# Optimization experiments

Hardware: AMD Instinct MI355X
Metric: run time of the kernel (lower is better)

## Reference

```python
import jax, jax.numpy as jnp
import numpy as np


def binarize(x):
    # sign-binarization to {-1, +1}; zeros map to -1, matching torch.where(tensor > 0, 1, -1)
    return jnp.where(x > 0, jnp.float32(1.0), jnp.float32(-1.0))


def setup_inputs() -> dict:
    key = jax.random.key(0)
    k1, k2, k3 = jax.random.split(key, 3)
    N, IN, OUT = 8192, 4096, 4096
    input = jax.random.normal(k1, (N, IN), dtype=jnp.float32)
    weight = jax.random.normal(k2, (IN, OUT), dtype=jnp.float32)  # [in_features, out_features]
    bias = jax.random.normal(k3, (OUT,), dtype=jnp.float32)
    return {"input": input, "weight": weight, "bias": bias}


def reference(input, weight, bias):
    # Binarize activations; quantized_weight is the binarized weight.
    x_b = binarize(input)            # [N, in]
    w_b = binarize(weight)           # [in, out]
    # XNOR/popcount GEMM over +-1 operands == plain matmul of the sign matrices.
    out = jnp.matmul(x_b, w_b) + bias  # [N, out]
    return out
```

## Files before the change

### kernel.cpp

```cpp
#include <hip/hip_runtime.h>
#include <stdint.h>


#define N_ROWS 8192
#define K_DIM  4096
#define O_DIM  4096
#define KW     64

typedef int   int4v    __attribute__((ext_vector_type(4)));
typedef int   int8v    __attribute__((ext_vector_type(8)));
typedef float float16v __attribute__((ext_vector_type(16)));

__device__ __forceinline__ int8v mk8u(int4v x) {
    return __builtin_shufflevector(x, x, 0, 1, 2, 3, -1, -1, -1, -1);
}

__device__ __forceinline__ uint32_t nib4(float f) { return f > 0.0f ? 0x2u : 0xAu; }

__global__ __launch_bounds__(256) void convert_xw_fp4(
        const float* __restrict__ X, const float* __restrict__ W,
        uint8_t* __restrict__ XB, uint8_t* __restrict__ WB) {
    int u    = blockIdx.x * 4 + (threadIdx.x >> 6);
    int lane = threadIdx.x & 63;

    if (u < 16384) {
        int g = u & 7, kt = (u >> 3) & 63, G = u >> 9;
        int row = G * 256 + g * 32 + (lane & 31);
        int k0  = kt * 64 + (lane >> 5) * 32;
        const float4* src = (const float4*)(X + (size_t)row * K_DIM + k0);
        uint32_t ow[4];
        #pragma unroll
        for (int q = 0; q < 4; ++q) {
            float4 vA = src[2 * q];
            float4 vB = src[2 * q + 1];
            uint32_t b0 = nib4(vA.x) | (nib4(vA.y) << 4);
            uint32_t b1 = nib4(vA.z) | (nib4(vA.w) << 4);
            uint32_t b2 = nib4(vB.x) | (nib4(vB.y) << 4);
            uint32_t b3 = nib4(vB.z) | (nib4(vB.w) << 4);
            ow[q] = b0 | (b1 << 8) | (b2 << 16) | (b3 << 24);
        }
        int4v o; o.x = (int)ow[0]; o.y = (int)ow[1]; o.z = (int)ow[2]; o.w = (int)ow[3];
        *(int4v*)(XB + (size_t)u * 1024 + lane * 16) = o;
    } else {
        int v = u - 16384;
        int g = v & 7, kt = (v >> 3) & 63, G = v >> 9;
        int o     = G * 256 + g * 32 + (lane & 31);
        int kbase = kt * 64 + (lane >> 5) * 32;
        const float* src = W + (size_t)kbase * O_DIM + o;
        uint32_t ow[4];
        #pragma unroll
        for (int q = 0; q < 4; ++q) {
            uint32_t x = 0;
            #pragma unroll
            for (int j = 0; j < 8; ++j) {
                float f = src[(size_t)(q * 8 + j) * O_DIM];
                x |= nib4(f) << (4 * j);
            }
            ow[q] = x;
        }
        int4v ov; ov.x = (int)ow[0]; ov.y = (int)ow[1]; ov.z = (int)ow[2]; ov.w = (int)ow[3];
        *(int4v*)(WB + (size_t)v * 1024 + lane * 16) = ov;
    }
}

#define MFMA4(a, b, c)                                                        \
    __builtin_amdgcn_mfma_scale_f32_32x32x64_f8f6f4(                          \
        (a), (b), (c), 4, 4, 0, 0x7F7F7F7F, 0, 0x7F7F7F7F)

__global__ __launch_bounds__(256, 2) void fp4_gemm_kernel(
        const uint8_t* __restrict__ XB, const uint8_t* __restrict__ WB,
        const float* __restrict__ bias, float* __restrict__ out) {
    __shared__ uint8_t lds[3 * 24576];

    const int tid  = threadIdx.x;
    const int swzb = (blockIdx.x & 7) * 128 + (blockIdx.x >> 3);
    const int brow = (swzb >> 5) * 256;
    const int bcol = (swzb & 31) * 128;

    const int lane = tid & 63;
    const int wid  = tid >> 6;
    const int wrow = (wid >> 1) * 128;
    const int wcol = (wid & 1) * 64;
    const int l31  = lane & 31;
    const int lh   = lane >> 5;

    const int ag0 = (wrow >> 5) * 1024 + lane * 16;
    const int bg0 = 16384 + (wcol >> 5) * 1024 + lane * 16;

    const uint8_t* Asrc = XB + ((size_t)(brow >> 8) << 19) + tid * 16;
    const uint8_t* Bsrc = WB + ((size_t)(bcol >> 8) << 19)
                             + ((bcol & 255) >> 5) * 1024 + tid * 16;

#define GSTAGE(buf, t)                                                        \
    {                                                                         \
        _Pragma("unroll")                                                     \
        for (int j = 0; j < 4; ++j) {                                         \
            __builtin_amdgcn_global_load_lds(                                 \
                (const __attribute__((address_space(1))) void*)               \
                    (Asrc + (size_t)(t) * 16384 + j * 4096),                  \
                (__attribute__((address_space(3))) void*)                     \
                    (lds + (buf) * 24576 + j * 4096 + tid * 16), 16, 0, 0);   \
        }                                                                     \
        _Pragma("unroll")                                                     \
        for (int h = 0; h < 2; ++h) {                                         \
            __builtin_amdgcn_global_load_lds(                                 \
                (const __attribute__((address_space(1))) void*)               \
                    (Bsrc + (size_t)(t) * 16384 + h * 8192),                  \
                (__attribute__((address_space(3))) void*)                     \
                    (lds + (buf) * 24576 + 16384 + h * 4096 + tid * 16),      \
                16, 0, 0);                                                    \
        }                                                                     \
    }

#define LOADH(A0, A1, A2, A3, B0, B1, buf, h)                                 \
    {                                                                         \
        const uint8_t* Ap = lds + (buf) * 24576 + (h) * 8192 + ag0;           \
        const uint8_t* Bp = lds + (buf) * 24576 + (h) * 4096 + bg0;           \
        A0 = mk8u(*(const int4v*)(Ap));                                       \
        A1 = mk8u(*(const int4v*)(Ap + 1024));                                \
        A2 = mk8u(*(const int4v*)(Ap + 2048));                                \
        A3 = mk8u(*(const int4v*)(Ap + 3072));                                \
        B0 = mk8u(*(const int4v*)(Bp));                                       \
        B1 = mk8u(*(const int4v*)(Bp + 1024));                                \
    }

#define MFMA8(A0, A1, A2, A3, B0, B1)                                         \
    {                                                                         \
        __builtin_amdgcn_s_setprio(1);                                        \
        c00 = MFMA4(A0, B0, c00);  c01 = MFMA4(A0, B1, c01);                  \
        c10 = MFMA4(A1, B0, c10);  c11 = MFMA4(A1, B1, c11);                  \
        c20 = MFMA4(A2, B0, c20);  c21 = MFMA4(A2, B1, c21);                  \
        c30 = MFMA4(A3, B0, c30);  c31 = MFMA4(A3, B1, c31);                  \
        __builtin_amdgcn_s_setprio(0);                                        \
    }

#define STEP(bufc, bufs, t, LASTWAIT)                                         \
    {                                                                         \
        if (LASTWAIT) asm volatile("s_waitcnt vmcnt(0)" ::: "memory");        \
        else          asm volatile("s_waitcnt vmcnt(6)" ::: "memory");        \
        __builtin_amdgcn_s_barrier();                                         \
        if ((t) + 2 < 32) GSTAGE(bufs, (t) + 2);                              \
        LOADH(a0, a1, a2, a3, b0, b1, bufc, 0);                               \
        LOADH(na0, na1, na2, na3, nb0, nb1, bufc, 1);                         \
        MFMA8(a0, a1, a2, a3, b0, b1);                                        \
        MFMA8(na0, na1, na2, na3, nb0, nb1);                                  \
    }

    float16v c00 = 0, c01 = 0, c10 = 0, c11 = 0,
             c20 = 0, c21 = 0, c30 = 0, c31 = 0;
    int8v a0, a1, a2, a3, b0, b1;
    int8v na0, na1, na2, na3, nb0, nb1;

    GSTAGE(0, 0);
    GSTAGE(1, 1);

    for (int i = 0; i < 10; ++i) {
        const int t = 3 * i;
        STEP(0, 2, t,     false);
        STEP(1, 0, t + 1, false);
        STEP(2, 1, t + 2, false);
    }
    STEP(0, 2, 30, false);
    STEP(1, 0, 31, true);
#undef STEP
#undef MFMA8
#undef LOADH
#undef GSTAGE

    float bv0 = bias[bcol + wcol + l31];
    float bv1 = bias[bcol + wcol + 32 + l31];
    const size_t obase = (size_t)(brow + wrow) * O_DIM + bcol + wcol;

#define CWRITE(cm, m, n, bv)                                                  \
    {                                                                         \
        _Pragma("unroll")                                                     \
        for (int r = 0; r < 16; ++r) {                                        \
            int rl = (r & 3) + 8 * (r >> 2) + 4 * lh;                         \
            out[obase + (size_t)((m) * 32 + rl) * O_DIM + (n) * 32 + l31] =   \
                cm[r] + (bv);                                                 \
        }                                                                     \
    }

    CWRITE(c00, 0, 0, bv0); CWRITE(c01, 0, 1, bv1);
    CWRITE(c10, 1, 0, bv0); CWRITE(c11, 1, 1, bv1);
    CWRITE(c20, 2, 0, bv0); CWRITE(c21, 2, 1, bv1);
    CWRITE(c30, 3, 0, bv0); CWRITE(c31, 3, 1, bv1);
#undef CWRITE
}

__global__ __launch_bounds__(256) void pack_x_kernel(
        const float* __restrict__ X, uint64_t* __restrict__ Xb) {
    int wave = (int)((blockIdx.x * blockDim.x + threadIdx.x) >> 6);
    int lane = threadIdx.x & 63;
    if (wave >= N_ROWS) return;
    const float* xr = X + (size_t)wave * K_DIM;
    uint64_t* xbr = Xb + (size_t)wave * KW;
    #pragma unroll 4
    for (int w = 0; w < KW; ++w) {
        float v = xr[w * 64 + lane];
        unsigned long long m = __ballot(v > 0.0f);
        if (lane == 0) xbr[w] = (uint64_t)m;
    }
}

__global__ __launch_bounds__(256) void pack_w_kernel(
        const float* __restrict__ W, uint64_t* __restrict__ Wb) {
    int oc = blockIdx.x & 15;
    int w  = blockIdx.x >> 4;
    int o  = oc * 256 + threadIdx.x;
    const float* wp = W + (size_t)(w * 64) * O_DIM + o;
    uint64_t word = 0;
    #pragma unroll 8
    for (int p = 0; p < 64; ++p) {
        float v = wp[(size_t)p * O_DIM];
        word |= (uint64_t)(v > 0.0f) << p;
    }
    Wb[(size_t)o * KW + w] = word;
}

__global__ __launch_bounds__(256) void xnor_gemm_kernel(
        const uint8_t* __restrict__ Xb, const uint8_t* __restrict__ Wb,
        const float* __restrict__ bias, float* __restrict__ out) {
    __shared__ uint4 lds4[2048];
    const int tid    = threadIdx.x;
    const int brow   = (blockIdx.x >> 5) * 128;
    const int bcol   = (blockIdx.x & 31) * 128;
    const int tx     = tid & 15;
    const int ty     = tid >> 4;
    const int widx   = tid >> 6;
    const int xbase0 = ty * 64 + (ty & 7);
    const int wbase0 = 1024 + tx * 64 + (tx & 7);
    uint32_t acc[8][8] = {};
    for (int kc = 0; kc < 4; ++kc) {
        __syncthreads();
        #pragma unroll
        for (int i = 0; i < 4; ++i) {
            int idx  = tid + 256 * i;
            int row  = idx >> 3;
            int srcc = (idx & 7) ^ ((idx >> 6) & 7);
            size_t goff = ((size_t)row << 9) + (kc << 7) + (srcc << 4);
            __builtin_amdgcn_global_load_lds(
                (const __attribute__((address_space(1))) void*)
                    (Xb + ((size_t)brow << 9) + goff),
                (__attribute__((address_space(3))) void*)
                    (lds4 + i * 256 + widx * 64), 16, 0, 0);
            __builtin_amdgcn_global_load_lds(
                (const __attribute__((address_space(1))) void*)
                    (Wb + ((size_t)bcol << 9) + goff),
                (__attribute__((address_space(3))) void*)
                    (lds4 + 1024 + i * 256 + widx * 64), 16, 0, 0);
        }
        asm volatile("s_waitcnt vmcnt(0)" ::: "memory");
        __syncthreads();
        for (int kq = 0; kq < 8; ++kq) {
            const uint4* xp = &lds4[xbase0 ^ kq];
            const uint4* wp = &lds4[wbase0 ^ kq];
            uint4 xq[8];
            #pragma unroll
            for (int r = 0; r < 8; ++r) xq[r] = xp[8 * r];
            #pragma unroll
            for (int c = 0; c < 8; ++c) {
                uint4 wv = wp[8 * c];
                #pragma unroll
                for (int r = 0; r < 8; ++r) {
                    uint32_t a = acc[r][c];
                    a = __builtin_popcount(xq[r].x ^ wv.x) + a;
                    a = __builtin_popcount(xq[r].y ^ wv.y) + a;
                    a = __builtin_popcount(xq[r].z ^ wv.z) + a;
                    a = __builtin_popcount(xq[r].w ^ wv.w) + a;
                    acc[r][c] = a;
                }
            }
        }
    }
    float bv[8];
    #pragma unroll
    for (int c = 0; c < 8; ++c) bv[c] = bias[bcol + tx * 8 + c];
    #pragma unroll
    for (int r = 0; r < 8; ++r) {
        float vals[8];
        #pragma unroll
        for (int c = 0; c < 8; ++c)
            vals[c] = (float)(K_DIM - 2 * (int)acc[r][c]) + bv[c];
        float4* op = (float4*)(out + (size_t)(brow + ty * 8 + r) * O_DIM
                               + bcol + tx * 8);
        op[0] = make_float4(vals[0], vals[1], vals[2], vals[3]);
        op[1] = make_float4(vals[4], vals[5], vals[6], vals[7]);
    }
}

extern "C" void kernel_launch(void* const* d_in, const int* in_sizes, int n_in,
                              void* d_out, int out_size, void* d_ws, size_t ws_size,
                              hipStream_t stream) {
    const float* X    = (const float*)d_in[0];
    const float* W    = (const float*)d_in[1];
    const float* bias = (const float*)d_in[2];
    float* out        = (float*)d_out;

    const size_t XB4 = (size_t)N_ROWS * K_DIM / 2;
    const size_t WB4 = (size_t)O_DIM * K_DIM / 2;

    if (ws_size >= XB4 + WB4) {
        uint8_t* XBlk = (uint8_t*)d_ws;
        uint8_t* WBlk = (uint8_t*)d_ws + XB4;

        convert_xw_fp4<<<(16384 + 8192) / 4, 256, 0, stream>>>(X, W, XBlk, WBlk);
        fp4_gemm_kernel<<<(N_ROWS / 256) * (O_DIM / 128), 256, 0, stream>>>(
            XBlk, WBlk, bias, out);
    } else {
        uint64_t* Xb = (uint64_t*)d_ws;
        uint64_t* Wb = (uint64_t*)((uint8_t*)d_ws + (size_t)N_ROWS * KW * 8);
        pack_x_kernel<<<N_ROWS / 4, 256, 0, stream>>>(X, Xb);
        pack_w_kernel<<<16 * 64, 256, 0, stream>>>(W, Wb);
        xnor_gemm_kernel<<<(N_ROWS / 128) * (O_DIM / 128), 256, 0, stream>>>(
            (const uint8_t*)Xb, (const uint8_t*)Wb, bias, out);
    }
}
```

Before: 126.2 us.

## Stage fp32 inputs through LDS with coalesced global_load_lds in FP4 conversion

The conversion kernel now stages tiles of X (32 rows x 512 k) and W (64 k x 256 cols) into shared memory with direct global-to-LDS loads that are fully coalesced, then reads each thread's slice out of LDS to pack the FP4 nibbles. Before, each lane read strided rows or strided columns straight from global memory, which coalesced poorly. The X tile uses a padded pitch to reduce bank conflicts. The W path still does column-strided LDS reads and may hit bank conflicts. The larger LDS footprint per block also lowers occupancy.

```diff
diff --git a/kernel.cpp b/kernel.cpp
--- a/kernel.cpp
+++ b/kernel.cpp
@@ -17,49 +17,103 @@
 
 __device__ __forceinline__ uint32_t nib4(float f) { return f > 0.0f ? 0x2u : 0xAu; }
 
+__device__ __forceinline__ uint32_t pack8(const float* f) {
+    uint32_t v = 0;
+    #pragma unroll
+    for (int j = 0; j < 8; ++j) v |= nib4(f[j]) << (4 * j);
+    return v;
+}
+
+#define XPITCH 2064
+
 __global__ __launch_bounds__(256) void convert_xw_fp4(
         const float* __restrict__ X, const float* __restrict__ W,
         uint8_t* __restrict__ XB, uint8_t* __restrict__ WB) {
-    int u    = blockIdx.x * 4 + (threadIdx.x >> 6);
-    int lane = threadIdx.x & 63;
-
-    if (u < 16384) {
-        int g = u & 7, kt = (u >> 3) & 63, G = u >> 9;
-        int row = G * 256 + g * 32 + (lane & 31);
-        int k0  = kt * 64 + (lane >> 5) * 32;
-        const float4* src = (const float4*)(X + (size_t)row * K_DIM + k0);
-        uint32_t ow[4];
-        #pragma unroll
-        for (int q = 0; q < 4; ++q) {
-            float4 vA = src[2 * q];
-            float4 vB = src[2 * q + 1];
-            uint32_t b0 = nib4(vA.x) | (nib4(vA.y) << 4);
-            uint32_t b1 = nib4(vA.z) | (nib4(vA.w) << 4);
-            uint32_t b2 = nib4(vB.x) | (nib4(vB.y) << 4);
-            uint32_t b3 = nib4(vB.z) | (nib4(vB.w) << 4);
-            ow[q] = b0 | (b1 << 8) | (b2 << 16) | (b3 << 24);
-        }
-        int4v o; o.x = (int)ow[0]; o.y = (int)ow[1]; o.z = (int)ow[2]; o.w = (int)ow[3];
-        *(int4v*)(XB + (size_t)u * 1024 + lane * 16) = o;
+    __shared__ uint8_t slds[32 * XPITCH];
+    const int tid  = threadIdx.x;
+    const int lane = tid & 63;
+    const int wid  = tid >> 6;
+
+    if (blockIdx.x < 2048) {
+        const int r0 = (blockIdx.x >> 3) * 32;
+        const int kq = blockIdx.x & 7;
+        const float* xs = X + (size_t)r0 * K_DIM + kq * 512;
+
+        #pragma unroll
+        for (int i = 0; i < 16; ++i) {
+            int p    = wid * 16 + i;
+            int row  = p >> 1;
+            int half = p & 1;
+            __builtin_amdgcn_global_load_lds(
+                (const __attribute__((address_space(1))) void*)
+                    (xs + (size_t)row * K_DIM + half * 256 + lane * 4),
+                (__attribute__((address_space(3))) void*)
+                    (slds + row * XPITCH + half * 1024 + lane * 16),
+                16, 0, 0);
+        }
+        asm volatile("s_waitcnt vmcnt(0)" ::: "memory");
+        __syncthreads();
+
+        const int row31 = lane & 31;
+        const int khalf = lane >> 5;
+        const int G = r0 >> 8, g = (r0 >> 5) & 7;
+        #pragma unroll
+        for (int i = 0; i < 2; ++i) {
+            int ktl = wid * 2 + i;
+            const float* src = (const float*)(slds + row31 * XPITCH
+                                              + (ktl * 64 + khalf * 32) * 4);
+            float fv[32];
+            #pragma unroll
+            for (int q = 0; q < 8; ++q)
+                *(float4*)(fv + 4 * q) = ((const float4*)src)[q];
+            uint32_t ow0 = pack8(fv), ow1 = pack8(fv + 8),
+                     ow2 = pack8(fv + 16), ow3 = pack8(fv + 24);
+            int4v o; o.x = (int)ow0; o.y = (int)ow1; o.z = (int)ow2; o.w = (int)ow3;
+            size_t base = ((size_t)G << 19) + (size_t)(kq * 8 + ktl) * 8192
+                        + (size_t)g * 1024;
+            *(int4v*)(XB + base + lane * 16) = o;
+        }
     } else {
-        int v = u - 16384;
-        int g = v & 7, kt = (v >> 3) & 63, G = v >> 9;
-        int o     = G * 256 + g * 32 + (lane & 31);
-        int kbase = kt * 64 + (lane >> 5) * 32;
-        const float* src = W + (size_t)kbase * O_DIM + o;
-        uint32_t ow[4];
-        #pragma unroll
-        for (int q = 0; q < 4; ++q) {
-            uint32_t x = 0;
+        const int wb = (int)blockIdx.x - 2048;
+        const int k0 = (wb >> 4) * 64;
+        const int o0 = (wb & 15) * 256;
+        const float* ws = W + (size_t)k0 * O_DIM + o0;
+
+        #pragma unroll
+        for (int i = 0; i < 16; ++i) {
+            int row = wid * 16 + i;
+            __builtin_amdgcn_global_load_lds(
+                (const __attribute__((address_space(1))) void*)
+                    (ws + (size_t)row * O_DIM + lane * 4),
+                (__attribute__((address_space(3))) void*)
+                    (slds + row * 1024 + lane * 16),
+                16, 0, 0);
+        }
+        asm volatile("s_waitcnt vmcnt(0)" ::: "memory");
+        __syncthreads();
+
+        const int o31   = lane & 31;
+        const int khalf = lane >> 5;
+        const int G = o0 >> 8, kt = k0 >> 6;
+        #pragma unroll
+        for (int i = 0; i < 2; ++i) {
+            int g = wid * 2 + i;
+            const uint8_t* col = slds + (khalf * 32) * 1024 + (g * 32 + o31) * 4;
+            uint32_t ow[4];
             #pragma unroll
-            for (int j = 0; j < 8; ++j) {
-                float f = src[(size_t)(q * 8 + j) * O_DIM];
-                x |= nib4(f) << (4 * j);
+            for (int q = 0; q < 4; ++q) {
+                uint32_t v = 0;
+                #pragma unroll
+                for (int j = 0; j < 8; ++j) {
+                    float f = *(const float*)(col + (q * 8 + j) * 1024);
+                    v |= nib4(f) << (4 * j);
+                }
+                ow[q] = v;
             }
-            ow[q] = x;
-        }
-        int4v ov; ov.x = (int)ow[0]; ov.y = (int)ow[1]; ov.z = (int)ow[2]; ov.w = (int)ow[3];
-        *(int4v*)(WB + (size_t)v * 1024 + lane * 16) = ov;
+            int4v o; o.x = (int)ow[0]; o.y = (int)ow[1]; o.z = (int)ow[2]; o.w = (int)ow[3];
+            size_t base = ((size_t)G << 19) + (size_t)kt * 8192 + (size_t)g * 1024;
+            *(int4v*)(WB + base + lane * 16) = o;
+        }
     }
 }
 
@@ -304,7 +358,7 @@
         uint8_t* XBlk = (uint8_t*)d_ws;
         uint8_t* WBlk = (uint8_t*)d_ws + XB4;
 
-        convert_xw_fp4<<<(16384 + 8192) / 4, 256, 0, stream>>>(X, W, XBlk, WBlk);
+        convert_xw_fp4<<<2048 + 1024, 256, 0, stream>>>(X, W, XBlk, WBlk);
         fp4_gemm_kernel<<<(N_ROWS / 256) * (O_DIM / 128), 256, 0, stream>>>(
             XBlk, WBlk, bias, out);
     } else {
```

Result: faster. 118.0 us (-6.5%).
